# Optimization experiments

Measured on AMD Instinct MI355X. Metric: run time of the kernel, lower is better.

Reference implementation:

```python
import jax, jax.numpy as jnp
import numpy as np

B, H, K, E = 8, 256, 256, 128
VOCAB, FVOCAB = 30000, 1000


def setup_inputs() -> dict:
    key = jax.random.key(0)
    k1, k2, k3, k4, k5, k6 = jax.random.split(key, 6)
    key_emb = jax.random.normal(k2, (VOCAB, E), dtype=jnp.float32)
    value_emb = jax.random.normal(k3, (FVOCAB, E), dtype=jnp.float32)
    # padding_idx=0 rows are zero
    key_emb = key_emb.at[0].set(0.0)
    value_emb = value_emb.at[0].set(0.0)
    return {
        "hidden": jax.random.normal(k1, (B, H, E), dtype=jnp.float32),
        "key_emb": key_emb,
        "value_emb": value_emb,
        "key_seq": jax.random.randint(k4, (B, K), 0, VOCAB, dtype=jnp.int64) if jax.config.jax_enable_x64 else jax.random.randint(k4, (B, K), 0, VOCAB).astype(jnp.int32),
        "value_seq": jax.random.randint(k5, (B, H, K), 0, FVOCAB).astype(jnp.int32),
        "mask_matrix": jax.random.randint(k6, (B, H, K), 0, 2).astype(jnp.int32),
    }


def reference(hidden, key_emb, value_emb, key_seq, value_seq, mask_matrix):
    scale = jnp.asarray(np.power(E, 0.5), dtype=jnp.float32)
    # embedding gathers (padding_idx=0 -> zero row, enforced in setup)
    k = key_emb[key_seq]            # [B, K, E]
    v = value_emb[value_seq]        # [B, H, K, E]
    # masked exp-normalize attention (manual, not softmax: no max-subtract)
    u = jnp.einsum('bhe,bke->bhk', hidden, k) / scale   # [B, H, K]
    delta = jnp.exp(u) * mask_matrix.astype(jnp.float32)
    p = delta / (jnp.sum(delta, axis=2, keepdims=True) + 1e-10)  # [B, H, K]
    # attention-weighted value aggregation
    o = jnp.einsum('bhk,bhke->bhe', p, v)               # [B, H, E]
    # nonzero-count averaging over H
    aspect_len = jnp.sum(o != 0, axis=1).astype(jnp.float32)     # [B, E]
    avg_o = jnp.sum(o, axis=1) / aspect_len                      # [B, E]
    return avg_o
```

## Files before the change

### kernel.cpp

```cpp
#include <hip/hip_runtime.h>
#include <math.h>

#define BB 8
#define HH 256
#define KK 256
#define EE 128

template <int CTRL, int RM>
__device__ __forceinline__ float dpp_add(float x) {
    int d = __builtin_amdgcn_update_dpp(0, __float_as_int(x), CTRL, RM, 0xf, true);
    return x + __int_as_float(d);
}
__device__ __forceinline__ float dpp_reduce_half(float x) {
    x = dpp_add<0x111, 0xf>(x);
    x = dpp_add<0x112, 0xf>(x);
    x = dpp_add<0x114, 0xf>(x);
    x = dpp_add<0x118, 0xf>(x);
    x = dpp_add<0x142, 0xa>(x);
    return x;
}
__device__ __forceinline__ float dpp_reduce_wave(float x) {
    x = dpp_reduce_half(x);
    x = dpp_add<0x143, 0xc>(x);
    return x;
}

__global__ __launch_bounds__(256) void kvmn_bh(
    const float* __restrict__ hidden,
    const float* __restrict__ key_emb,
    const float* __restrict__ value_emb,
    const int*   __restrict__ key_seq,
    const int*   __restrict__ value_seq,
    const int*   __restrict__ mask,
    float* __restrict__ o_ws)
{
    __shared__ float  sh_u[KK];
    __shared__ float  sh_part[4];
    __shared__ float4 sh_o4[8][32];

    const int bid  = blockIdx.x;
    const int b    = bid >> 8;
    const int h    = bid & 255;
    const int tid  = threadIdx.x;
    const int w    = tid >> 6;
    const int lane = tid & 63;
    const int half = lane >> 5;
    const int sub  = lane & 31;

    const int ksreg = key_seq[b * KK + tid];
    const int vsreg = value_seq[(size_t)(b * HH + h) * KK + tid];
    const int my_mask = mask[(size_t)(b * HH + h) * KK + tid];

    const float4 h4 = *(const float4*)&hidden[(size_t)(b * HH + h) * EE + sub * 4];

    const float inv_scale = 0.08838834764831845f;

    #pragma unroll 16
    for (int i = 0; i < 32; ++i) {
        const int    row = __shfl(ksreg, half * 32 + i, 64);
        const float4 kv  = *(const float4*)&key_emb[(size_t)row * EE + sub * 4];
        float part = kv.x * h4.x + kv.y * h4.y + kv.z * h4.z + kv.w * h4.w;
        part = dpp_reduce_half(part);
        if (sub == 31) sh_u[w * 64 + half * 32 + i] = part * inv_scale;
    }
    __syncthreads();

    const float d = expf(sh_u[tid]) * (float)my_mask;
    float s = dpp_reduce_wave(d);
    if (lane == 63) sh_part[w] = s;
    __syncthreads();
    const float denom = sh_part[0] + sh_part[1] + sh_part[2] + sh_part[3];
    const float pk = d * (1.0f / (denom + 1e-10f));

    float4 acc = make_float4(0.f, 0.f, 0.f, 0.f);
    #pragma unroll 16
    for (int i = 0; i < 32; ++i) {
        const int    src = half * 32 + i;
        const float  p   = __shfl(pk, src, 64);
        const int    row = __shfl(vsreg, src, 64);
        const float4 v   = *(const float4*)&value_emb[(size_t)row * EE + sub * 4];
        acc.x += p * v.x;
        acc.y += p * v.y;
        acc.z += p * v.z;
        acc.w += p * v.w;
    }
    sh_o4[w * 2 + half][sub] = acc;
    __syncthreads();

    if (tid < 32) {
        float4 t = sh_o4[0][tid];
        #pragma unroll
        for (int r = 1; r < 8; ++r) {
            const float4 q = sh_o4[r][tid];
            t.x += q.x; t.y += q.y; t.z += q.z; t.w += q.w;
        }
        *(float4*)&o_ws[(size_t)(b * HH + h) * EE + tid * 4] = t;
    }
}

__global__ __launch_bounds__(256) void kvmn_reduce(
    const float* __restrict__ o_ws,
    float* __restrict__ out)
{
    __shared__ float sh_sum[256];
    __shared__ int   sh_cnt[256];

    const int b  = blockIdx.x;
    const int t  = threadIdx.x;
    const int e  = t & 127;
    const int hh = t >> 7;

    float sum = 0.0f;
    int   cnt = 0;
    const float* base = o_ws + (size_t)(b * HH + hh * 128) * EE + e;
    #pragma unroll 8
    for (int h = 0; h < 128; ++h) {
        const float v = base[(size_t)h * EE];
        sum += v;
        cnt += (v != 0.0f) ? 1 : 0;
    }
    sh_sum[t] = sum;
    sh_cnt[t] = cnt;
    __syncthreads();
    if (t < 128) {
        const float s = sh_sum[t] + sh_sum[t + 128];
        const int   c = sh_cnt[t] + sh_cnt[t + 128];
        out[b * EE + t] = s / (float)c;
    }
}

extern "C" void kernel_launch(void* const* d_in, const int* in_sizes, int n_in,
                              void* d_out, int out_size, void* d_ws, size_t ws_size,
                              hipStream_t stream) {
    const float* hidden    = (const float*)d_in[0];
    const float* key_emb   = (const float*)d_in[1];
    const float* value_emb = (const float*)d_in[2];
    const int*   key_seq   = (const int*)d_in[3];
    const int*   value_seq = (const int*)d_in[4];
    const int*   mask      = (const int*)d_in[5];

    float* o_ws = (float*)d_ws;

    kvmn_bh<<<BB * HH, 256, 0, stream>>>(hidden, key_emb, value_emb,
                                         key_seq, value_seq, mask, o_ws);
    kvmn_reduce<<<BB, 256, 0, stream>>>(o_ws, (float*)d_out);
    (void)in_sizes; (void)n_in; (void)out_size; (void)ws_size;
}
```

Baseline: 102.2 us.

## Replace value gathers with per-batch probability histogram over value vocabulary

Because the sum over H of attention outputs equals a weighted sum of value embedding rows, each block scatters its attention probabilities into a shared-memory histogram indexed by value id instead of gathering value rows. A finalize kernel merges the histograms per batch and multiplies them by the small value table. Each block now handles four H rows, so every key embedding gather is reused four times. The nonzero count becomes a per-row test for any unmasked nonzero value id, which matches the reference only when such rows give fully nonzero outputs. The finalize stage runs on just eight blocks, which may serialize.

```diff
diff --git a/kernel.cpp b/kernel.cpp
--- a/kernel.cpp
+++ b/kernel.cpp
@@ -5,6 +5,9 @@
 #define HH 256
 #define KK 256
 #define EE 128
+#define HJ 4
+#define NBLK (BB * HH / HJ)
+#define NBIN 1024
 
 template <int CTRL, int RM>
 __device__ __forceinline__ float dpp_add(float x) {
@@ -25,22 +28,23 @@
     return x;
 }
 
-__global__ __launch_bounds__(256) void kvmn_bh(
+__global__ __launch_bounds__(256) void kvmn_attn_hist(
     const float* __restrict__ hidden,
     const float* __restrict__ key_emb,
-    const float* __restrict__ value_emb,
     const int*   __restrict__ key_seq,
     const int*   __restrict__ value_seq,
     const int*   __restrict__ mask,
-    float* __restrict__ o_ws)
+    float* __restrict__ part_hist,
+    int*   __restrict__ c_part)
 {
-    __shared__ float  sh_u[KK];
-    __shared__ float  sh_part[4];
-    __shared__ float4 sh_o4[8][32];
+    __shared__ float sh_u[HJ][KK];
+    __shared__ float hist[NBIN];
+    __shared__ float fslot[HJ][4];
+    __shared__ int   islot[HJ][4];
 
     const int bid  = blockIdx.x;
-    const int b    = bid >> 8;
-    const int h    = bid & 255;
+    const int b    = bid >> 6;
+    const int h0   = (bid & 63) * HJ;
     const int tid  = threadIdx.x;
     const int w    = tid >> 6;
     const int lane = tid & 63;
@@ -48,85 +52,105 @@
     const int sub  = lane & 31;
 
     const int ksreg = key_seq[b * KK + tid];
-    const int vsreg = value_seq[(size_t)(b * HH + h) * KK + tid];
-    const int my_mask = mask[(size_t)(b * HH + h) * KK + tid];
 
-    const float4 h4 = *(const float4*)&hidden[(size_t)(b * HH + h) * EE + sub * 4];
+    float4 h4[HJ];
+    #pragma unroll
+    for (int j = 0; j < HJ; ++j)
+        h4[j] = *(const float4*)&hidden[(size_t)(b * HH + h0 + j) * EE + sub * 4];
+
+    *(float4*)&hist[tid * 4] = make_float4(0.f, 0.f, 0.f, 0.f);
 
     const float inv_scale = 0.08838834764831845f;
 
-    #pragma unroll 16
+    #pragma unroll 8
     for (int i = 0; i < 32; ++i) {
         const int    row = __shfl(ksreg, half * 32 + i, 64);
         const float4 kv  = *(const float4*)&key_emb[(size_t)row * EE + sub * 4];
-        float part = kv.x * h4.x + kv.y * h4.y + kv.z * h4.z + kv.w * h4.w;
-        part = dpp_reduce_half(part);
-        if (sub == 31) sh_u[w * 64 + half * 32 + i] = part * inv_scale;
+        const int    k2  = w * 64 + half * 32 + i;
+        #pragma unroll
+        for (int j = 0; j < HJ; ++j) {
+            float part = kv.x * h4[j].x + kv.y * h4[j].y + kv.z * h4[j].z + kv.w * h4[j].w;
+            part = dpp_reduce_half(part);
+            if (sub == 31) sh_u[j][k2] = part * inv_scale;
+        }
     }
     __syncthreads();
 
-    const float d = expf(sh_u[tid]) * (float)my_mask;
-    float s = dpp_reduce_wave(d);
-    if (lane == 63) sh_part[w] = s;
-    __syncthreads();
-    const float denom = sh_part[0] + sh_part[1] + sh_part[2] + sh_part[3];
-    const float pk = d * (1.0f / (denom + 1e-10f));
-
-    float4 acc = make_float4(0.f, 0.f, 0.f, 0.f);
-    #pragma unroll 16
-    for (int i = 0; i < 32; ++i) {
-        const int    src = half * 32 + i;
-        const float  p   = __shfl(pk, src, 64);
-        const int    row = __shfl(vsreg, src, 64);
-        const float4 v   = *(const float4*)&value_emb[(size_t)row * EE + sub * 4];
-        acc.x += p * v.x;
-        acc.y += p * v.y;
-        acc.z += p * v.z;
-        acc.w += p * v.w;
+    float d[HJ];
+    int   vs[HJ];
+    #pragma unroll
+    for (int j = 0; j < HJ; ++j) {
+        const size_t idx = (size_t)(b * HH + h0 + j) * KK + tid;
+        const int m = mask[idx];
+        vs[j] = value_seq[idx];
+        d[j]  = expf(sh_u[j][tid]) * (float)m;
+        const float s = dpp_reduce_wave(d[j]);
+        if (lane == 63) fslot[j][w] = s;
+        const int any = __any(m != 0 && vs[j] != 0);
+        if (lane == 0) islot[j][w] = any ? 1 : 0;
     }
-    sh_o4[w * 2 + half][sub] = acc;
     __syncthreads();
 
-    if (tid < 32) {
-        float4 t = sh_o4[0][tid];
+    #pragma unroll
+    for (int j = 0; j < HJ; ++j) {
+        const float denom = fslot[j][0] + fslot[j][1] + fslot[j][2] + fslot[j][3];
+        const float p = d[j] * (1.0f / (denom + 1e-10f));
+        atomicAdd(&hist[vs[j]], p);
+    }
+    if (tid == 0) {
+        int c = 0;
         #pragma unroll
-        for (int r = 1; r < 8; ++r) {
-            const float4 q = sh_o4[r][tid];
-            t.x += q.x; t.y += q.y; t.z += q.z; t.w += q.w;
-        }
-        *(float4*)&o_ws[(size_t)(b * HH + h) * EE + tid * 4] = t;
+        for (int j = 0; j < HJ; ++j)
+            c += (islot[j][0] | islot[j][1] | islot[j][2] | islot[j][3]);
+        c_part[bid] = c;
     }
+    __syncthreads();
+
+    *(float4*)&part_hist[(size_t)bid * NBIN + tid * 4] = *(float4*)&hist[tid * 4];
 }
 
-__global__ __launch_bounds__(256) void kvmn_reduce(
-    const float* __restrict__ o_ws,
+__global__ __launch_bounds__(512) void kvmn_finalize(
+    const float* __restrict__ part_hist,
+    const int*   __restrict__ c_part,
+    const float* __restrict__ value_emb,
     float* __restrict__ out)
 {
-    __shared__ float sh_sum[256];
-    __shared__ int   sh_cnt[256];
+    __shared__ float H[NBIN];
+    __shared__ float gs[4][EE];
+    __shared__ int   csh[64];
+    __shared__ float cval;
 
-    const int b  = blockIdx.x;
-    const int t  = threadIdx.x;
-    const int e  = t & 127;
-    const int hh = t >> 7;
+    const int b   = blockIdx.x;
+    const int tid = threadIdx.x;
 
-    float sum = 0.0f;
-    int   cnt = 0;
-    const float* base = o_ws + (size_t)(b * HH + hh * 128) * EE + e;
+    float2 acc2 = make_float2(0.f, 0.f);
     #pragma unroll 8
-    for (int h = 0; h < 128; ++h) {
-        const float v = base[(size_t)h * EE];
-        sum += v;
-        cnt += (v != 0.0f) ? 1 : 0;
+    for (int i = 0; i < 64; ++i) {
+        const float2 v = *(const float2*)&part_hist[(size_t)(b * 64 + i) * NBIN + tid * 2];
+        acc2.x += v.x;
+        acc2.y += v.y;
     }
-    sh_sum[t] = sum;
-    sh_cnt[t] = cnt;
+    *(float2*)&H[tid * 2] = acc2;
+    if (tid < 64) csh[tid] = c_part[b * 64 + tid];
     __syncthreads();
-    if (t < 128) {
-        const float s = sh_sum[t] + sh_sum[t + 128];
-        const int   c = sh_cnt[t] + sh_cnt[t + 128];
-        out[b * EE + t] = s / (float)c;
+    if (tid == 0) {
+        int c = 0;
+        #pragma unroll
+        for (int i = 0; i < 64; ++i) c += csh[i];
+        cval = (float)c;
     }
+
+    const int e  = tid & 127;
+    const int qt = tid >> 7;
+    float acc = 0.f;
+    const int bin0 = qt * 250;
+    #pragma unroll 5
+    for (int bin = bin0; bin < bin0 + 250; ++bin)
+        acc += H[bin] * value_emb[(size_t)bin * EE + e];
+    gs[qt][e] = acc;
+    __syncthreads();
+    if (tid < 128)
+        out[b * EE + tid] = (gs[0][tid] + gs[1][tid] + gs[2][tid] + gs[3][tid]) / cval;
 }
 
 extern "C" void kernel_launch(void* const* d_in, const int* in_sizes, int n_in,
@@ -139,10 +163,11 @@
     const int*   value_seq = (const int*)d_in[4];
     const int*   mask      = (const int*)d_in[5];
 
-    float* o_ws = (float*)d_ws;
+    float* part_hist = (float*)d_ws;
+    int*   c_part    = (int*)((char*)d_ws + (size_t)NBLK * NBIN * 4);
 
-    kvmn_bh<<<BB * HH, 256, 0, stream>>>(hidden, key_emb, value_emb,
-                                         key_seq, value_seq, mask, o_ws);
-    kvmn_reduce<<<BB, 256, 0, stream>>>(o_ws, (float*)d_out);
+    kvmn_attn_hist<<<NBLK, 256, 0, stream>>>(hidden, key_emb, key_seq,
+                                             value_seq, mask, part_hist, c_part);
+    kvmn_finalize<<<BB, 512, 0, stream>>>(part_hist, c_part, value_emb, (float*)d_out);
     (void)in_sizes; (void)n_in; (void)out_size; (void)ws_size;
 }
```

Measured after the change: 115.5 us. 1.13x slower.

## Replace value gather with per-row probability histogram over value vocabulary

Applied to the files above, without the earlier changes.

Instead of gathering a value-embedding row for every (b,h,k) entry, each (b,h) block scatters its attention weights into a shared-memory histogram over the 1000-entry value vocabulary. A separate reduce kernel sums the histograms over H and multiplies once by value_emb. Key rows are pre-gathered into a transposed per-batch buffer so score computation reads them coalesced. The nonzero count is replaced by a per-row ballot flag: a row counts if any unmasked entry has a nonzero value index. This assumes a row's output is either fully nonzero or fully zero, which holds for generic embeddings. The cost is an 8 MB partial-histogram round trip through global memory and shared-memory atomics.

```diff
diff --git a/kernel.cpp b/kernel.cpp
--- a/kernel.cpp
+++ b/kernel.cpp
@@ -5,38 +5,55 @@
 #define HH 256
 #define KK 256
 #define EE 128
+#define E4 (EE / 4)
+#define NBIN 1024
+#define NBH (BB * HH)
 
 template <int CTRL, int RM>
 __device__ __forceinline__ float dpp_add(float x) {
     int d = __builtin_amdgcn_update_dpp(0, __float_as_int(x), CTRL, RM, 0xf, true);
     return x + __int_as_float(d);
 }
-__device__ __forceinline__ float dpp_reduce_half(float x) {
+__device__ __forceinline__ float dpp_reduce_wave(float x) {
     x = dpp_add<0x111, 0xf>(x);
     x = dpp_add<0x112, 0xf>(x);
     x = dpp_add<0x114, 0xf>(x);
     x = dpp_add<0x118, 0xf>(x);
     x = dpp_add<0x142, 0xa>(x);
-    return x;
-}
-__device__ __forceinline__ float dpp_reduce_wave(float x) {
-    x = dpp_reduce_half(x);
     x = dpp_add<0x143, 0xc>(x);
     return x;
 }
 
-__global__ __launch_bounds__(256) void kvmn_bh(
-    const float* __restrict__ hidden,
+__global__ __launch_bounds__(256) void kvmn_gather(
     const float* __restrict__ key_emb,
-    const float* __restrict__ value_emb,
     const int*   __restrict__ key_seq,
-    const int*   __restrict__ value_seq,
-    const int*   __restrict__ mask,
-    float* __restrict__ o_ws)
+    float4* __restrict__ KgT,
+    float*  __restrict__ sum_ws,
+    int*    __restrict__ c_ws)
 {
-    __shared__ float  sh_u[KK];
-    __shared__ float  sh_part[4];
-    __shared__ float4 sh_o4[8][32];
+    const int g  = blockIdx.x * 256 + threadIdx.x;
+    const int b  = g >> 13;
+    const int e4 = (g >> 8) & 31;
+    const int k  = g & 255;
+    const int row = key_seq[b * KK + k];
+    const float4 v = *(const float4*)&key_emb[(size_t)row * EE + e4 * 4];
+    KgT[((size_t)b * E4 + e4) * KK + k] = v;
+    if (g < BB * EE) sum_ws[g] = 0.0f;
+    if (g < BB)      c_ws[g]   = 0;
+}
+
+__global__ __launch_bounds__(256) void kvmn_attn(
+    const float*  __restrict__ hidden,
+    const float4* __restrict__ KgT,
+    const int*    __restrict__ value_seq,
+    const int*    __restrict__ mask,
+    float* __restrict__ part_hist,
+    int*   __restrict__ c_ws)
+{
+    __shared__ float4 sh_h[E4];
+    __shared__ float  hist[NBIN];
+    __shared__ float  fslot[4];
+    __shared__ int    islot[4];
 
     const int bid  = blockIdx.x;
     const int b    = bid >> 8;
@@ -44,89 +61,92 @@
     const int tid  = threadIdx.x;
     const int w    = tid >> 6;
     const int lane = tid & 63;
-    const int half = lane >> 5;
-    const int sub  = lane & 31;
 
-    const int ksreg = key_seq[b * KK + tid];
-    const int vsreg = value_seq[(size_t)(b * HH + h) * KK + tid];
-    const int my_mask = mask[(size_t)(b * HH + h) * KK + tid];
+    if (tid < E4)
+        sh_h[tid] = *(const float4*)&hidden[((size_t)b * HH + h) * EE + tid * 4];
+    *(float4*)&hist[tid * 4] = make_float4(0.f, 0.f, 0.f, 0.f);
 
-    const float4 h4 = *(const float4*)&hidden[(size_t)(b * HH + h) * EE + sub * 4];
+    const size_t idx = ((size_t)b * HH + h) * KK + tid;
+    const int m  = mask[idx];
+    const int vs = value_seq[idx];
+    __syncthreads();
 
-    const float inv_scale = 0.08838834764831845f;
+    const float4* kcol = KgT + (size_t)b * E4 * KK + tid;
+    float acc = 0.0f;
+    #pragma unroll 8
+    for (int e4 = 0; e4 < E4; ++e4) {
+        const float4 kv = kcol[(size_t)e4 * KK];
+        const float4 hv = sh_h[e4];
+        acc += kv.x * hv.x + kv.y * hv.y + kv.z * hv.z + kv.w * hv.w;
+    }
 
-    #pragma unroll 16
-    for (int i = 0; i < 32; ++i) {
-        const int    row = __shfl(ksreg, half * 32 + i, 64);
-        const float4 kv  = *(const float4*)&key_emb[(size_t)row * EE + sub * 4];
-        float part = kv.x * h4.x + kv.y * h4.y + kv.z * h4.z + kv.w * h4.w;
-        part = dpp_reduce_half(part);
-        if (sub == 31) sh_u[w * 64 + half * 32 + i] = part * inv_scale;
+    const float d = expf(acc * 0.08838834764831845f) * (float)m;
+    const float s = dpp_reduce_wave(d);
+    if (lane == 63) fslot[w] = s;
+    const unsigned long long bal = __ballot(m != 0 && vs != 0);
+    if (lane == 0) islot[w] = (bal != 0ull) ? 1 : 0;
+    __syncthreads();
+    const float denom = fslot[0] + fslot[1] + fslot[2] + fslot[3];
+    const float p = d * (1.0f / (denom + 1e-10f));
+
+    atomicAdd(&hist[vs], p);
+    if (tid == 0) {
+        const int f = islot[0] | islot[1] | islot[2] | islot[3];
+        if (f) atomicAdd(&c_ws[b], 1);
     }
     __syncthreads();
 
-    const float d = expf(sh_u[tid]) * (float)my_mask;
-    float s = dpp_reduce_wave(d);
-    if (lane == 63) sh_part[w] = s;
+    *(float4*)&part_hist[(size_t)bid * NBIN + tid * 4] = *(float4*)&hist[tid * 4];
+}
+
+__global__ __launch_bounds__(256) void kvmn_hreduce(
+    const float* __restrict__ part_hist,
+    const float* __restrict__ value_emb,
+    float* __restrict__ sum_ws)
+{
+    __shared__ float Hsh[2][128];
+    __shared__ float gs[2][128];
+
+    const int bid  = blockIdx.x;
+    const int b    = bid >> 3;
+    const int c    = bid & 7;
+    const int t    = threadIdx.x;
+    const int binl = t & 127;
+    const int hh   = t >> 7;
+
+    float s = 0.0f;
+    const float* base = part_hist + ((size_t)(b * HH) + hh * 128) * NBIN + c * 128 + binl;
+    #pragma unroll 8
+    for (int i = 0; i < 128; ++i)
+        s += base[(size_t)i * NBIN];
+    Hsh[hh][binl] = s;
     __syncthreads();
-    const float denom = sh_part[0] + sh_part[1] + sh_part[2] + sh_part[3];
-    const float pk = d * (1.0f / (denom + 1e-10f));
-
-    float4 acc = make_float4(0.f, 0.f, 0.f, 0.f);
-    #pragma unroll 16
-    for (int i = 0; i < 32; ++i) {
-        const int    src = half * 32 + i;
-        const float  p   = __shfl(pk, src, 64);
-        const int    row = __shfl(vsreg, src, 64);
-        const float4 v   = *(const float4*)&value_emb[(size_t)row * EE + sub * 4];
-        acc.x += p * v.x;
-        acc.y += p * v.y;
-        acc.z += p * v.z;
-        acc.w += p * v.w;
-    }
-    sh_o4[w * 2 + half][sub] = acc;
+    if (t < 128) Hsh[0][t] = Hsh[0][t] + Hsh[1][t];
     __syncthreads();
 
-    if (tid < 32) {
-        float4 t = sh_o4[0][tid];
-        #pragma unroll
-        for (int r = 1; r < 8; ++r) {
-            const float4 q = sh_o4[r][tid];
-            t.x += q.x; t.y += q.y; t.z += q.z; t.w += q.w;
-        }
-        *(float4*)&o_ws[(size_t)(b * HH + h) * EE + tid * 4] = t;
+    const int e  = binl;
+    const int rr = hh;
+    float acc = 0.0f;
+    #pragma unroll 8
+    for (int j = 0; j < 64; ++j) {
+        const int gb = c * 128 + rr * 64 + j;
+        if (gb < 1000)
+            acc += Hsh[0][rr * 64 + j] * value_emb[(size_t)gb * EE + e];
     }
+    gs[rr][e] = acc;
+    __syncthreads();
+    if (t < 128)
+        atomicAdd(&sum_ws[b * EE + t], gs[0][t] + gs[1][t]);
 }
 
-__global__ __launch_bounds__(256) void kvmn_reduce(
-    const float* __restrict__ o_ws,
+__global__ __launch_bounds__(128) void kvmn_div(
+    const float* __restrict__ sum_ws,
+    const int*   __restrict__ c_ws,
     float* __restrict__ out)
 {
-    __shared__ float sh_sum[256];
-    __shared__ int   sh_cnt[256];
-
-    const int b  = blockIdx.x;
-    const int t  = threadIdx.x;
-    const int e  = t & 127;
-    const int hh = t >> 7;
-
-    float sum = 0.0f;
-    int   cnt = 0;
-    const float* base = o_ws + (size_t)(b * HH + hh * 128) * EE + e;
-    #pragma unroll 8
-    for (int h = 0; h < 128; ++h) {
-        const float v = base[(size_t)h * EE];
-        sum += v;
-        cnt += (v != 0.0f) ? 1 : 0;
-    }
-    sh_sum[t] = sum;
-    sh_cnt[t] = cnt;
-    __syncthreads();
-    if (t < 128) {
-        const float s = sh_sum[t] + sh_sum[t + 128];
-        const int   c = sh_cnt[t] + sh_cnt[t + 128];
-        out[b * EE + t] = s / (float)c;
-    }
+    const int b = blockIdx.x;
+    const int t = threadIdx.x;
+    out[b * EE + t] = sum_ws[b * EE + t] / (float)c_ws[b];
 }
 
 extern "C" void kernel_launch(void* const* d_in, const int* in_sizes, int n_in,
@@ -139,10 +159,15 @@
     const int*   value_seq = (const int*)d_in[4];
     const int*   mask      = (const int*)d_in[5];
 
-    float* o_ws = (float*)d_ws;
+    char* ws = (char*)d_ws;
+    float4* KgT       = (float4*)ws;
+    float*  part_hist = (float*)(ws + (1u << 20));
+    float*  sum_ws    = (float*)(ws + (9u << 20));
+    int*    c_ws      = (int*)  (ws + (9u << 20) + 4096);
 
-    kvmn_bh<<<BB * HH, 256, 0, stream>>>(hidden, key_emb, value_emb,
-                                         key_seq, value_seq, mask, o_ws);
-    kvmn_reduce<<<BB, 256, 0, stream>>>(o_ws, (float*)d_out);
+    kvmn_gather <<<BB * KK * E4 / 256, 256, 0, stream>>>(key_emb, key_seq, KgT, sum_ws, c_ws);
+    kvmn_attn   <<<NBH, 256, 0, stream>>>(hidden, KgT, value_seq, mask, part_hist, c_ws);
+    kvmn_hreduce<<<64, 256, 0, stream>>>(part_hist, value_emb, sum_ws);
+    kvmn_div    <<<BB, 128, 0, stream>>>(sum_ws, c_ws, (float*)d_out);
     (void)in_sizes; (void)n_in; (void)out_size; (void)ws_size;
 }
```

Result: slower. 131.2 us (+28.4%).
